# Kernel optimization log

Hardware: AMD Instinct MI355X
Metric: run time of the kernel (lower is better)

## Reference

```python
import jax, jax.numpy as jnp
import numpy as np
import math

N, E, MUL = 10000, 160000, 128
D = MUL * 4  # 128x0e (128) + 128x1o (384) = 512
NEURONS = 32
EDGE_ATTR_DIM = 32
WEIGHT_NUMEL = 4 * MUL  # 4 uvu tensor-product paths, 128 weights each


def ssp(x):
    return jax.nn.softplus(x) - math.log(2.0)


def irrep_linear(x, W0, b0, W1):
    # o3.Linear on 128x0e+128x1o: mixes mul channels within each irrep, fan-in normalized,
    # bias only on scalar (0e) block.
    s = x[:, :MUL] @ (W0 / jnp.sqrt(MUL)) + b0
    v = x[:, MUL:].reshape(-1, MUL, 3)
    v = jnp.einsum('num,uv->nvm', v, W1) / jnp.sqrt(MUL)
    return jnp.concatenate([s, v.reshape(-1, MUL * 3)], axis=-1)


def inner_product(a, b):
    # InnerProduct: uuu channel-wise irrep inner product, 1/sqrt(dim) normalized
    s = a[:, :MUL] * b[:, :MUL]
    va = a[:, MUL:].reshape(-1, MUL, 3)
    vb = b[:, MUL:].reshape(-1, MUL, 3)
    v = jnp.einsum('num,num->nu', va, vb) / jnp.sqrt(3.0)
    return jnp.concatenate([s, v], axis=-1)


def norm_gate(x, W1, b1, W2, b2):
    # NormGate: per-channel norms of l>0 irreps -> MLP gates -> gate l>0 channels
    v = x[:, MUL:].reshape(-1, MUL, 3)
    norm_v = jnp.sqrt(jnp.sum(v * v, axis=-1) + 1e-12)      # [n, 128]
    f0 = jnp.concatenate([x[:, :MUL], norm_v], axis=-1)     # [n, 256]
    g = jax.nn.silu(f0 @ W1 + b1) @ W2 + b2                 # [n, 256]
    gated = v * g[:, MUL:, None]
    return jnp.concatenate([g[:, :MUL], gated.reshape(-1, MUL * 3)], axis=-1)


def mlp2(x, Wa, Wb):
    # e3nn FullyConnectedNet: fan-in normalized, ssp nonlinearity on hidden layer only
    return ssp(x @ (Wa / jnp.sqrt(Wa.shape[0]))) @ (Wb / jnp.sqrt(Wb.shape[0]))


def setup_inputs():
    key = jax.random.key(0)
    ks = jax.random.split(key, 20)
    r = lambda i, shp: jax.random.normal(ks[i], shp, dtype=jnp.float32)
    return {
        'x': r(0, (N, D)),
        'edge_index': jax.random.randint(ks[1], (2, E), 0, N, dtype=jnp.int32),
        'edge_attr': jax.random.uniform(ks[2], (E, EDGE_ATTR_DIM), dtype=jnp.float32),
        'edge_sh': r(3, (E, 4)),
        'Wp0': r(4, (MUL, MUL)), 'bp0': jnp.zeros((MUL,), jnp.float32), 'Wp1': r(5, (MUL, MUL)),
        'ngW1': r(6, (2 * MUL, 2 * MUL)) / 16.0, 'ngb1': jnp.zeros((2 * MUL,), jnp.float32),
        'ngW2': r(7, (2 * MUL, 2 * MUL)) / 16.0, 'ngb2': jnp.zeros((2 * MUL,), jnp.float32),
        'Wn0': r(8, (MUL, MUL)), 'bn0': jnp.zeros((MUL,), jnp.float32), 'Wn1': r(9, (MUL, MUL)),
        'fcnW1': r(10, (EDGE_ATTR_DIM, NEURONS)), 'fcnW2': r(11, (NEURONS, WEIGHT_NUMEL)),
        'l0W1': r(12, (3 * MUL, NEURONS)), 'l0W2': r(13, (NEURONS, WEIGHT_NUMEL)),
        'Wo0': r(14, (MUL, MUL)), 'bo0': jnp.zeros((MUL,), jnp.float32), 'Wo1': r(15, (MUL, MUL)),
    }


def reference(x, edge_index, edge_attr, edge_sh, Wp0, bp0, Wp1, ngW1, ngb1, ngW2, ngb2,
              Wn0, bn0, Wn1, fcnW1, fcnW2, l0W1, l0W2, Wo0, bo0, Wo1):
    edge_dst, edge_src = edge_index[0], edge_index[1]
    # invariant edge descriptor s0 from pre-linear + inner product
    pre_x = irrep_linear(x, Wp0, bp0, Wp1)
    ip = inner_product(pre_x[edge_dst], pre_x[edge_src])[:, MUL:]             # [E,128]
    s0 = jnp.concatenate([pre_x[edge_dst][:, :MUL], pre_x[edge_src][:, :MUL], ip], axis=-1)  # [E,384]
    # norm-gate + linear on node features
    x = norm_gate(x, ngW1, ngb1, ngW2, ngb2)
    x = irrep_linear(x, Wn0, bn0, Wn1)
    self_x = x
    # per-edge tensor-product weights: fc_node(edge_attr) * layer_l0(s0)
    w = mlp2(edge_attr, fcnW1, fcnW2) * mlp2(s0, l0W1, l0W2)                   # [E,512]
    w1, w2, w3, w4 = w[:, :MUL], w[:, MUL:2 * MUL], w[:, 2 * MUL:3 * MUL], w[:, 3 * MUL:]
    xs = x[edge_src]
    xs0 = xs[:, :MUL]                     # [E,128]
    xs1 = xs[:, MUL:].reshape(E, MUL, 3)  # [E,128,3]
    sh0 = edge_sh[:, 0:1]
    sh1 = edge_sh[:, 1:4]
    # uvu CG tensor product paths: 0ex0e->0e, 0ex1o->1o, 1ox0e->1o, 1ox1o->0e
    c0, c1 = 0.5, jnp.sqrt(3.0) / 2.0  # path norm sqrt(ir_out.dim / n_paths)
    out0 = c0 * (w1 * xs0 * sh0 + w4 * jnp.einsum('eum,em->eu', xs1, sh1) / jnp.sqrt(3.0))
    out1 = c1 * (w2[:, :, None] * xs0[:, :, None] * sh1[:, None, :]
                 + w3[:, :, None] * xs1 * sh0[:, :, None])
    edge_feat = jnp.concatenate([out0, out1.reshape(E, MUL * 3)], axis=-1)     # [E,512]
    # scatter-aggregate to destination nodes, residual, output linear
    out = jax.ops.segment_sum(edge_feat, edge_dst, num_segments=N)
    out = out + self_x
    return irrep_linear(out, Wo0, bo0, Wo1)
```

## Files before the change

kernel.cpp:

```cpp
#include <hip/hip_runtime.h>
#include <hip/hip_fp16.h>
#include <math.h>

#define NN 10000
#define EE 160000
#define DPB 8

#define RS128 0.08838834764831845f
#define RS384 0.05103103630798287f
#define RS32  0.17677669529663687f
#define R3    0.57735026918962576f
#define C1V   0.86602540378443865f

typedef _Float16 half8 __attribute__((ext_vector_type(8)));
typedef _Float16 half4 __attribute__((ext_vector_type(4)));
typedef float f32x4 __attribute__((ext_vector_type(4)));

__device__ __forceinline__ float sspf(float x) {
    return fmaxf(x, 0.0f) + log1pf(__expf(-fabsf(x))) - 0.69314718055994530942f;
}

__device__ __forceinline__ void packone(const float* __restrict__ W,
                                        _Float16* __restrict__ P,
                                        int K, int N, int off) {
    const int KS = K >> 5;
    int j = off & 7, lane = (off >> 3) & 63, rest = off >> 9;
    int ks = rest % KS, ct = rest / KS;
    int k = ks * 32 + ((lane >> 4) << 3) + j;
    int c = ct * 16 + (lane & 15);
    P[off] = (_Float16)W[k * N + c];
}

__global__ __launch_bounds__(256) void k_packall(
    const float* __restrict__ Wp0, const float* __restrict__ Wp1,
    const float* __restrict__ Wn0, const float* __restrict__ Wn1,
    const float* __restrict__ Wo0, const float* __restrict__ Wo1,
    const float* __restrict__ ngW1, const float* __restrict__ ngW2,
    const float* __restrict__ l0W1, const float* __restrict__ fcnW1,
    const float* __restrict__ fcnW2, const float* __restrict__ l0W2,
    _Float16* __restrict__ pWp0, _Float16* __restrict__ pWp1,
    _Float16* __restrict__ pWn0, _Float16* __restrict__ pWn1,
    _Float16* __restrict__ pWo0, _Float16* __restrict__ pWo1,
    _Float16* __restrict__ png1, _Float16* __restrict__ png2,
    _Float16* __restrict__ pWc, _Float16* __restrict__ pWa,
    _Float16* __restrict__ Wf_t, _Float16* __restrict__ Wl_t) {
    int idx = blockIdx.x * 256 + threadIdx.x;
    if (idx < 98304) {
        int seg = idx >> 14, off = idx & 16383;
        if (seg == 0) packone(Wp0, pWp0, 128, 128, off);
        else if (seg == 1) packone(Wp1, pWp1, 128, 128, off);
        else if (seg == 2) packone(Wn0, pWn0, 128, 128, off);
        else if (seg == 3) packone(Wn1, pWn1, 128, 128, off);
        else if (seg == 4) packone(Wo0, pWo0, 128, 128, off);
        else packone(Wo1, pWo1, 128, 128, off);
    } else if (idx < 229376) {
        int r = idx - 98304;
        if (r < 65536) packone(ngW1, png1, 256, 256, r);
        else packone(ngW2, png2, 256, 256, r - 65536);
    } else if (idx < 233472) {
        packone(l0W1 + 256 * 32, pWc, 128, 32, idx - 229376);
    } else if (idx < 234496) {
        packone(fcnW1, pWa, 32, 32, idx - 233472);
    } else {
        int off = idx - 234496;
        int k = off & 31, c = off >> 5;
        Wf_t[c * 32 + k] = (_Float16)fcnW2[k * 512 + c];
        Wl_t[c * 32 + k] = (_Float16)l0W2[k * 512 + c];
    }
}

__global__ __launch_bounds__(256) void k_irrep_m(
    const float* __restrict__ X, const _Float16* __restrict__ pW0,
    const float* __restrict__ b0, const _Float16* __restrict__ pW1,
    float* __restrict__ out) {
    __shared__ _Float16 Xr[4][16][136];
    const int t = threadIdx.x, lane = t & 63, w = t >> 6;
    const int nb = blockIdx.x * 16;
    for (int idx = t; idx < 16 * 128; idx += 256) {
        int n = idx >> 7, c4 = idx & 127;
        const float4 v = *(const float4*)(X + (size_t)(nb + n) * 512 + 4 * c4);
        float vals[4] = {v.x, v.y, v.z, v.w};
        int c = 4 * c4;
#pragma unroll
        for (int j = 0; j < 4; ++j) {
            int cc = c + j;
            if (cc < 128) Xr[0][n][cc] = (_Float16)vals[j];
            else { int d = cc - 128; Xr[1 + d % 3][n][d / 3] = (_Float16)vals[j]; }
        }
    }
    __syncthreads();
    const _Float16* pW = (w == 0) ? pW0 : pW1;
    const int row16 = lane & 15, kg = lane >> 4;
    f32x4 acc[8];
    const f32x4 zero = {0.0f, 0.0f, 0.0f, 0.0f};
#pragma unroll
    for (int ct = 0; ct < 8; ++ct) acc[ct] = zero;
    for (int ks = 0; ks < 4; ++ks) {
        const half8 a = *(const half8*)&Xr[w][row16][ks * 32 + kg * 8];
#pragma unroll
        for (int ct = 0; ct < 8; ++ct) {
            const half8 b = *(const half8*)(pW + (((ct * 4 + ks) * 64 + lane) << 3));
            acc[ct] = __builtin_amdgcn_mfma_f32_16x16x32_f16(a, b, acc[ct], 0, 0, 0);
        }
    }
#pragma unroll
    for (int ct = 0; ct < 8; ++ct) {
        const int col = ct * 16 + row16;
        const float bb = (w == 0) ? b0[col] : 0.0f;
#pragma unroll
        for (int r = 0; r < 4; ++r) {
            const int node = nb + kg * 4 + r;
            const float val = acc[ct][r] * RS128 + bb;
            if (w == 0) out[(size_t)node * 512 + col] = val;
            else out[(size_t)node * 512 + 128 + 3 * col + (w - 1)] = val;
        }
    }
}

__global__ __launch_bounds__(256) void k_self_m(
    const float* __restrict__ X,
    const _Float16* __restrict__ png1, const float* __restrict__ ngb1,
    const _Float16* __restrict__ png2, const float* __restrict__ ngb2,
    const _Float16* __restrict__ pWn0, const float* __restrict__ bn0,
    const _Float16* __restrict__ pWn1,
    _Float16* __restrict__ selfx_h) {
    __shared__ _Float16 f0h[16][264];
    __shared__ _Float16 t1h[16][264];
    __shared__ _Float16 xvh[3][16][136];
    const int t = threadIdx.x, lane = t & 63, w = t >> 6;
    const int nb = blockIdx.x * 16;
    const int row16 = lane & 15, kg = lane >> 4;
    const f32x4 zero = {0.0f, 0.0f, 0.0f, 0.0f};

    for (int idx = t; idx < 16 * 128; idx += 256) {
        int n = idx >> 7, c4 = idx & 127;
        const float4 v = *(const float4*)(X + (size_t)(nb + n) * 512 + 4 * c4);
        float vals[4] = {v.x, v.y, v.z, v.w};
        int c = 4 * c4;
#pragma unroll
        for (int j = 0; j < 4; ++j) {
            int cc = c + j;
            if (cc < 128) f0h[n][cc] = (_Float16)vals[j];
            else { int d = cc - 128; xvh[d % 3][n][d / 3] = (_Float16)vals[j]; }
        }
    }
    __syncthreads();
    for (int idx = t; idx < 16 * 128; idx += 256) {
        int n = idx >> 7, u = idx & 127;
        float a = (float)xvh[0][n][u], b = (float)xvh[1][n][u], c = (float)xvh[2][n][u];
        f0h[n][128 + u] = (_Float16)sqrtf(fmaf(a, a, fmaf(b, b, fmaf(c, c, 1e-12f))));
    }
    __syncthreads();
    {
        f32x4 acc[4];
#pragma unroll
        for (int i = 0; i < 4; ++i) acc[i] = zero;
        for (int ks = 0; ks < 8; ++ks) {
            const half8 a = *(const half8*)&f0h[row16][ks * 32 + kg * 8];
#pragma unroll
            for (int c2 = 0; c2 < 4; ++c2) {
                const int ct = 4 * w + c2;
                const half8 b = *(const half8*)(png1 + (((ct * 8 + ks) * 64 + lane) << 3));
                acc[c2] = __builtin_amdgcn_mfma_f32_16x16x32_f16(a, b, acc[c2], 0, 0, 0);
            }
        }
#pragma unroll
        for (int c2 = 0; c2 < 4; ++c2) {
            const int col = (4 * w + c2) * 16 + row16;
            const float bb = ngb1[col];
#pragma unroll
            for (int r = 0; r < 4; ++r) {
                const float z = acc[c2][r] + bb;
                t1h[kg * 4 + r][col] = (_Float16)(z / (1.0f + __expf(-z)));
            }
        }
    }
    __syncthreads();
    {
        f32x4 acc[4];
#pragma unroll
        for (int i = 0; i < 4; ++i) acc[i] = zero;
        for (int ks = 0; ks < 8; ++ks) {
            const half8 a = *(const half8*)&t1h[row16][ks * 32 + kg * 8];
#pragma unroll
            for (int c2 = 0; c2 < 4; ++c2) {
                const int ct = 4 * w + c2;
                const half8 b = *(const half8*)(png2 + (((ct * 8 + ks) * 64 + lane) << 3));
                acc[c2] = __builtin_amdgcn_mfma_f32_16x16x32_f16(a, b, acc[c2], 0, 0, 0);
            }
        }
        __syncthreads();
#pragma unroll
        for (int c2 = 0; c2 < 4; ++c2) {
            const int col = (4 * w + c2) * 16 + row16;
            const float bb = ngb2[col];
#pragma unroll
            for (int r = 0; r < 4; ++r)
                f0h[kg * 4 + r][col] = (_Float16)(acc[c2][r] + bb);
        }
    }
    __syncthreads();
    for (int idx = t; idx < 16 * 128; idx += 256) {
        int n = idx >> 7, u = idx & 127;
        const _Float16 g = f0h[n][128 + u];
        xvh[0][n][u] = xvh[0][n][u] * g;
        xvh[1][n][u] = xvh[1][n][u] * g;
        xvh[2][n][u] = xvh[2][n][u] * g;
    }
    __syncthreads();
    {
        const _Float16* pw = (w == 0) ? pWn0 : pWn1;
        f32x4 acc[8];
#pragma unroll
        for (int ct = 0; ct < 8; ++ct) acc[ct] = zero;
        for (int ks = 0; ks < 4; ++ks) {
            const half8 a = (w == 0)
                ? *(const half8*)&f0h[row16][ks * 32 + kg * 8]
                : *(const half8*)&xvh[w - 1][row16][ks * 32 + kg * 8];
#pragma unroll
            for (int ct = 0; ct < 8; ++ct) {
                const half8 b = *(const half8*)(pw + (((ct * 4 + ks) * 64 + lane) << 3));
                acc[ct] = __builtin_amdgcn_mfma_f32_16x16x32_f16(a, b, acc[ct], 0, 0, 0);
            }
        }
#pragma unroll
        for (int ct = 0; ct < 8; ++ct) {
            const int col = ct * 16 + row16;
            const float bb = (w == 0) ? bn0[col] : 0.0f;
#pragma unroll
            for (int r = 0; r < 4; ++r) {
                const int n = kg * 4 + r;
                const float val = acc[ct][r] * RS128 + bb;
                if (w == 0) f0h[n][col] = (_Float16)val;
                else xvh[w - 1][n][col] = (_Float16)val;
            }
        }
    }
    __syncthreads();
    for (int idx = t; idx < 16 * 128; idx += 256) {
        int n = idx >> 7, u = idx & 127;
        half4 sx = {f0h[n][u], xvh[0][n][u], xvh[1][n][u], xvh[2][n][u]};
        *(half4*)(selfx_h + (size_t)(nb + n) * 512 + (u << 2)) = sx;
    }
}

__global__ __launch_bounds__(256) void k_pre(
    const float* __restrict__ prex, const float* __restrict__ l0W1,
    float* __restrict__ pAB) {
    __shared__ float xs[8][128];
    const int t = threadIdx.x;
    const int nb = blockIdx.x * 8;
    for (int idx = t; idx < 8 * 128; idx += 256) {
        int n = idx >> 7, u = idx & 127;
        xs[n][u] = prex[(size_t)(nb + n) * 512 + u];
    }
    __syncthreads();
    const int n = t >> 5, k = t & 31;
    float a = 0, b = 0;
    for (int u = 0; u < 128; ++u) {
        float s = xs[n][u];
        a = fmaf(s, l0W1[u * 32 + k], a);
        b = fmaf(s, l0W1[(128 + u) * 32 + k], b);
    }
    pAB[(size_t)(nb + n) * 64 + k] = a;
    pAB[(size_t)(nb + n) * 64 + 32 + k] = b;
}

__global__ __launch_bounds__(256) void k_deg(const int* __restrict__ ei, int* __restrict__ deg) {
    int e = blockIdx.x * 256 + threadIdx.x;
    if (e < EE) atomicAdd(&deg[ei[e]], 1);
}

__global__ __launch_bounds__(1024) void k_scan(const int* __restrict__ deg, int* __restrict__ row_ptr) {
    __shared__ int part[1024];
    const int t = threadIdx.x;
    const int base = t * 10;
    int loc[10];
    int s = 0;
#pragma unroll
    for (int i = 0; i < 10; ++i) {
        int idx = base + i;
        int d = (idx < NN) ? deg[idx] : 0;
        loc[i] = s;
        s += d;
    }
    part[t] = s;
    __syncthreads();
    for (int off = 1; off < 1024; off <<= 1) {
        int v = (t >= off) ? part[t - off] : 0;
        __syncthreads();
        part[t] += v;
        __syncthreads();
    }
    int excl = (t > 0) ? part[t - 1] : 0;
#pragma unroll
    for (int i = 0; i < 10; ++i) {
        int idx = base + i;
        if (idx <= NN) row_ptr[idx] = excl + loc[i];
    }
}

__global__ __launch_bounds__(256) void k_fill(const int* __restrict__ ei,
                                              const int* __restrict__ row_ptr,
                                              int* __restrict__ cursor,
                                              int* __restrict__ csr_eid) {
    int e = blockIdx.x * 256 + threadIdx.x;
    if (e < EE) {
        int d = ei[e];
        int pos = atomicAdd(&cursor[d], 1);
        csr_eid[row_ptr[d] + pos] = e;
    }
}

__global__ __launch_bounds__(256) void k_hidden_m(
    const float* __restrict__ prex, const float* __restrict__ pAB,
    const int* __restrict__ edge_index, const float* __restrict__ edge_attr,
    const int* __restrict__ csr_eid,
    const _Float16* __restrict__ pWc, const _Float16* __restrict__ pWa,
    __half* __restrict__ hh) {
    const int pb = blockIdx.x * 32;
    const int t = threadIdx.x, lane = t & 63, w = t >> 6;
    __shared__ _Float16 ipl[32][132];
    __shared__ _Float16 eal[32][36];
    __shared__ _Float16 h1o[32][32];
    __shared__ _Float16 hao[32][32];
    __shared__ int dsts[32], srcs[32], eids[32];

    if (t < 32) {
        const int id = csr_eid[pb + t];
        eids[t] = id;
        dsts[t] = edge_index[id];
        srcs[t] = edge_index[EE + id];
    }
    __syncthreads();
    for (int idx = t; idx < 32 * 32; idx += 256) {
        int e = idx >> 5, j = idx & 31;
        eal[e][j] = (_Float16)edge_attr[(size_t)eids[e] * 32 + j];
    }
    for (int idx = t; idx < 32 * 128; idx += 256) {
        int e = idx >> 7, u = idx & 127;
        const float* pd = prex + (size_t)dsts[e] * 512 + 128 + 3 * u;
        const float* ps = prex + (size_t)srcs[e] * 512 + 128 + 3 * u;
        ipl[e][u] = (_Float16)((pd[0] * ps[0] + pd[1] * ps[1] + pd[2] * ps[2]) * R3);
    }
    __syncthreads();

    const int row16 = lane & 15, kg = lane >> 4;
    const int mt = w >> 1, ct = w & 1;
    const int e0 = mt * 16;
    const f32x4 zero = {0.0f, 0.0f, 0.0f, 0.0f};
    const int kc = ct * 16 + row16;

    {
        f32x4 acc = zero;
#pragma unroll
        for (int ks = 0; ks < 4; ++ks) {
            const half8 a = *(const half8*)&ipl[e0 + row16][ks * 32 + kg * 8];
            const half8 b = *(const half8*)(pWc + (((ct * 4 + ks) * 64 + lane) << 3));
            acc = __builtin_amdgcn_mfma_f32_16x16x32_f16(a, b, acc, 0, 0, 0);
        }
#pragma unroll
        for (int r = 0; r < 4; ++r) {
            const int e = e0 + kg * 4 + r;
            const float v = acc[r] + pAB[(size_t)dsts[e] * 64 + kc]
                                   + pAB[(size_t)srcs[e] * 64 + 32 + kc];
            h1o[e][kc] = (_Float16)sspf(v * RS384);
        }
    }
    {
        const half8 a = *(const half8*)&eal[e0 + row16][kg * 8];
        const half8 b = *(const half8*)(pWa + ((ct * 64 + lane) << 3));
        f32x4 acc = __builtin_amdgcn_mfma_f32_16x16x32_f16(a, b, zero, 0, 0, 0);
#pragma unroll
        for (int r = 0; r < 4; ++r) {
            const int e = e0 + kg * 4 + r;
            hao[e][kc] = (_Float16)sspf((float)acc[r] * RS32);
        }
    }
    __syncthreads();
    for (int idx = t; idx < 32 * 32; idx += 256) {
        const int e = idx >> 5, j = idx & 31;
        unsigned vv;
        if (j < 16) {
            __half2 h2 = __halves2half2((__half)h1o[e][2 * j], (__half)h1o[e][2 * j + 1]);
            vv = *(unsigned*)&h2;
        } else {
            const int jj = j - 16;
            __half2 h2 = __halves2half2((__half)hao[e][2 * jj], (__half)hao[e][2 * jj + 1]);
            vv = *(unsigned*)&h2;
        }
        ((unsigned*)hh)[(size_t)(pb + e) * 32 + j] = vv;
    }
}

__global__ __launch_bounds__(512) void k_accum(
    const __half* __restrict__ hh, const _Float16* __restrict__ selfx_h,
    const int* __restrict__ edge_index, const float* __restrict__ edge_sh,
    const int* __restrict__ row_ptr, const int* __restrict__ csr_eid,
    const _Float16* __restrict__ Wf_t, const _Float16* __restrict__ Wl_t,
    float* __restrict__ outacc) {
    const int dst0 = blockIdx.x * DPB;
    const int t = threadIdx.x;
    const int lane = t & 63;
    const int wid = t >> 6;
    const int lcol = lane & 15;
    const int kg = lane >> 4;
    const int u = 16 * wid + lcol;
    const int koff = kg * 8;

    __shared__ __align__(16) _Float16 h1s[2][4][16][8];
    __shared__ __align__(16) _Float16 has[2][4][16][8];
    __shared__ float shl[2][16][4];
    __shared__ int cbeg[DPB], cne[DPB], cchk[DPB + 1];

    if (t < DPB) {
        const int b = row_ptr[dst0 + t];
        cbeg[t] = b;
        cne[t] = row_ptr[dst0 + t + 1] - b;
    }
    __syncthreads();
    if (t == 0) {
        int s = 0;
#pragma unroll
        for (int i = 0; i < DPB; ++i) { cchk[i] = s; s += max(1, (cne[i] + 15) >> 4); }
        cchk[DPB] = s;
    }
    half8 bf[4], bl[4];
#pragma unroll
    for (int q = 0; q < 4; ++q) {
        const int col = q * 128 + u;
        bf[q] = *(const half8*)(Wf_t + col * 32 + koff);
        bl[q] = *(const half8*)(Wl_t + col * 32 + koff);
    }
    __syncthreads();
    const int nc = cchk[DPB];
    const float inv32 = 1.0f / 32.0f;

    float acc0 = 0, acc1 = 0, acc2 = 0, acc3 = 0;

    unsigned rhh = 0;
    float4 rsh = {0.0f, 0.0f, 0.0f, 0.0f};
    const half4 h4z = {(_Float16)0, (_Float16)0, (_Float16)0, (_Float16)0};
    half4 nsx[4] = {h4z, h4z, h4z, h4z};
    half4 csx[4];

    const int se = t >> 5, sw = t & 31;

    auto issue = [&](int ci) {
        int dd = 0;
        while (dd + 1 < DPB && ci >= cchk[dd + 1]) ++dd;
        const int c0 = (ci - cchk[dd]) << 4;
        const int ce = min(16, cne[dd] - c0);
        const int pos = cbeg[dd] + c0;
        rhh = (se < ce) ? ((const unsigned*)hh)[(size_t)(pos + se) * 32 + sw] : 0u;
        if (t < 16) {
            if (t < ce) {
                const int id = csr_eid[pos + t];
                rsh = *(const float4*)(edge_sh + (size_t)id * 4);
            } else {
                rsh = make_float4(0.0f, 0.0f, 0.0f, 0.0f);
            }
        }
#pragma unroll
        for (int r = 0; r < 4; ++r) {
            const int e = kg * 4 + r;
            if (e < ce) {
                const int id2 = csr_eid[pos + e];
                const int s = edge_index[EE + id2];
                nsx[r] = *(const half4*)(selfx_h + (size_t)s * 512 + (u << 2));
            } else {
                nsx[r] = h4z;
            }
        }
    };

    auto flush = [&](int dd) {
        acc0 += __shfl_xor(acc0, 16, 64); acc0 += __shfl_xor(acc0, 32, 64);
        acc1 += __shfl_xor(acc1, 16, 64); acc1 += __shfl_xor(acc1, 32, 64);
        acc2 += __shfl_xor(acc2, 16, 64); acc2 += __shfl_xor(acc2, 32, 64);
        acc3 += __shfl_xor(acc3, 16, 64); acc3 += __shfl_xor(acc3, 32, 64);
        if (lane < 16) {
            const size_t g = (size_t)(dst0 + dd) * 512;
            const half4 sx = *(const half4*)(selfx_h + g + (u << 2));
            outacc[g + u] = acc0 + (float)sx.x;
            outacc[g + 128 + 3 * u + 0] = acc1 + (float)sx.y;
            outacc[g + 128 + 3 * u + 1] = acc2 + (float)sx.z;
            outacc[g + 128 + 3 * u + 2] = acc3 + (float)sx.w;
        }
        acc0 = acc1 = acc2 = acc3 = 0;
    };

    issue(0);
    int cur = 0, cur_dd = 0;
    for (int ci = 0; ci < nc; ++ci) {
        if (sw < 16) ((unsigned*)h1s[cur])[(sw >> 2) * 64 + se * 4 + (sw & 3)] = rhh;
        else         ((unsigned*)has[cur])[((sw - 16) >> 2) * 64 + se * 4 + ((sw - 16) & 3)] = rhh;
        if (t < 16) {
            shl[cur][t][0] = rsh.x; shl[cur][t][1] = rsh.y;
            shl[cur][t][2] = rsh.z; shl[cur][t][3] = rsh.w;
        }
#pragma unroll
        for (int r = 0; r < 4; ++r) csx[r] = nsx[r];
        int dd = 0;
        while (dd + 1 < DPB && ci >= cchk[dd + 1]) ++dd;
        if (ci + 1 < nc) issue(ci + 1);
        __syncthreads();
        if (dd != cur_dd) { flush(cur_dd); cur_dd = dd; }

        const half8 haf = *(const half8*)(&has[cur][kg][lcol][0]);
        const half8 h1f = *(const half8*)(&h1s[cur][kg][lcol][0]);
        const f32x4 zero = {0.0f, 0.0f, 0.0f, 0.0f};
        f32x4 A[4], B[4];
#pragma unroll
        for (int q = 0; q < 4; ++q) {
            A[q] = __builtin_amdgcn_mfma_f32_16x16x32_f16(haf, bf[q], zero, 0, 0, 0);
            B[q] = __builtin_amdgcn_mfma_f32_16x16x32_f16(h1f, bl[q], zero, 0, 0, 0);
        }
#pragma unroll
        for (int r = 0; r < 4; ++r) {
            const int e = kg * 4 + r;
            const float w1 = A[0][r] * B[0][r] * inv32;
            const float w2 = A[1][r] * B[1][r] * inv32;
            const float w3 = A[2][r] * B[2][r] * inv32;
            const float w4 = A[3][r] * B[3][r] * inv32;
            const float sh0 = shl[cur][e][0], s1x = shl[cur][e][1];
            const float s1y = shl[cur][e][2], s1z = shl[cur][e][3];
            const float xs0 = (float)csx[r].x;
            const float xv0 = (float)csx[r].y;
            const float xv1 = (float)csx[r].z;
            const float xv2 = (float)csx[r].w;
            const float dv = xv0 * s1x + xv1 * s1y + xv2 * s1z;
            acc0 += 0.5f * (w1 * xs0 * sh0 + w4 * dv * R3);
            acc1 += C1V * (w2 * xs0 * s1x + w3 * xv0 * sh0);
            acc2 += C1V * (w2 * xs0 * s1y + w3 * xv1 * sh0);
            acc3 += C1V * (w2 * xs0 * s1z + w3 * xv2 * sh0);
        }
        cur ^= 1;
    }
    flush(cur_dd);
}

extern "C" void kernel_launch(void* const* d_in, const int* in_sizes, int n_in,
                              void* d_out, int out_size, void* d_ws, size_t ws_size,
                              hipStream_t stream) {
    const float* x = (const float*)d_in[0];
    const int* edge_index = (const int*)d_in[1];
    const float* edge_attr = (const float*)d_in[2];
    const float* edge_sh = (const float*)d_in[3];
    const float* Wp0 = (const float*)d_in[4];
    const float* bp0 = (const float*)d_in[5];
    const float* Wp1 = (const float*)d_in[6];
    const float* ngW1 = (const float*)d_in[7];
    const float* ngb1 = (const float*)d_in[8];
    const float* ngW2 = (const float*)d_in[9];
    const float* ngb2 = (const float*)d_in[10];
    const float* Wn0 = (const float*)d_in[11];
    const float* bn0 = (const float*)d_in[12];
    const float* Wn1 = (const float*)d_in[13];
    const float* fcnW1 = (const float*)d_in[14];
    const float* fcnW2 = (const float*)d_in[15];
    const float* l0W1 = (const float*)d_in[16];
    const float* l0W2 = (const float*)d_in[17];
    const float* Wo0 = (const float*)d_in[18];
    const float* bo0 = (const float*)d_in[19];
    const float* Wo1 = (const float*)d_in[20];

    float* out = (float*)d_out;
    float* prex = out;
    _Float16* selfx_h = (_Float16*)d_ws;
    int* deg = (int*)(selfx_h + (size_t)NN * 512);
    int* cursor = deg + NN;
    int* row_ptr = cursor + NN;
    int* csr_eid = row_ptr + NN + 1;
    float* pAB = (float*)(csr_eid + EE);
    __half* hh = (__half*)(pAB + (size_t)NN * 64);
    _Float16* Wf_t = (_Float16*)(hh + (size_t)EE * 64);
    _Float16* Wl_t = Wf_t + 512 * 32;
    _Float16* pWp0 = Wl_t + 512 * 32;
    _Float16* pWp1 = pWp0 + 128 * 128;
    _Float16* pWn0 = pWp1 + 128 * 128;
    _Float16* pWn1 = pWn0 + 128 * 128;
    _Float16* pWo0 = pWn1 + 128 * 128;
    _Float16* pWo1 = pWo0 + 128 * 128;
    _Float16* png1 = pWo1 + 128 * 128;
    _Float16* png2 = png1 + 256 * 256;
    _Float16* pWc  = png2 + 256 * 256;
    _Float16* pWa  = pWc + 128 * 32;

    hipMemsetAsync(deg, 0, 2 * NN * sizeof(int), stream);

    k_packall<<<980, 256, 0, stream>>>(Wp0, Wp1, Wn0, Wn1, Wo0, Wo1, ngW1, ngW2,
                                       l0W1, fcnW1, fcnW2, l0W2,
                                       pWp0, pWp1, pWn0, pWn1, pWo0, pWo1,
                                       png1, png2, pWc, pWa, Wf_t, Wl_t);

    k_irrep_m<<<NN / 16, 256, 0, stream>>>(x, pWp0, bp0, pWp1, prex);
    k_pre<<<NN / 8, 256, 0, stream>>>(prex, l0W1, pAB);
    k_self_m<<<NN / 16, 256, 0, stream>>>(x, png1, ngb1, png2, ngb2, pWn0, bn0, pWn1,
                                          selfx_h);
    k_deg<<<EE / 256, 256, 0, stream>>>(edge_index, deg);
    k_scan<<<1, 1024, 0, stream>>>(deg, row_ptr);
    k_fill<<<EE / 256, 256, 0, stream>>>(edge_index, row_ptr, cursor, csr_eid);
    k_hidden_m<<<EE / 32, 256, 0, stream>>>(prex, pAB, edge_index, edge_attr, csr_eid,
                                            pWc, pWa, hh);
    k_accum<<<NN / DPB, 512, 0, stream>>>(hh, selfx_h, edge_index, edge_sh, row_ptr, csr_eid,
                                          Wf_t, Wl_t, out);
    k_irrep_m<<<NN / 16, 256, 0, stream>>>(out, pWo0, bo0, pWo1, out);
}
```

Measured before the change: 299.4 us.

## Prefetch source indices two chunks ahead and broadcast them via shuffles

Breaks the dependent index chain (csr_eid, then edge_index, then the selfx gather) into stages. Lanes 0-15 load the source node index for the chunk two steps ahead, and the row gather for the next chunk uses __shfl to broadcast those indices. This replaces the per-lane redundant dependent index loads and hides their latency. Out-of-range edges now gather node 0 and are masked in the compute loop, at the cost of extra branching and register pressure.

```diff
diff --git a/kernel.cpp b/kernel.cpp
--- a/kernel.cpp
+++ b/kernel.cpp
@@ -440,18 +440,23 @@
 
     unsigned rhh = 0;
     float4 rsh = {0.0f, 0.0f, 0.0f, 0.0f};
+    int ridx = 0;
     const half4 h4z = {(_Float16)0, (_Float16)0, (_Float16)0, (_Float16)0};
     half4 nsx[4] = {h4z, h4z, h4z, h4z};
     half4 csx[4];
 
     const int se = t >> 5, sw = t & 31;
 
-    auto issue = [&](int ci) {
+    auto chunkmeta = [&](int ci, int& pos, int& ce) {
         int dd = 0;
         while (dd + 1 < DPB && ci >= cchk[dd + 1]) ++dd;
         const int c0 = (ci - cchk[dd]) << 4;
-        const int ce = min(16, cne[dd] - c0);
-        const int pos = cbeg[dd] + c0;
+        ce = min(16, cne[dd] - c0);
+        pos = cbeg[dd] + c0;
+    };
+
+    auto issue_meta = [&](int ci) {
+        int pos, ce; chunkmeta(ci, pos, ce);
         rhh = (se < ce) ? ((const unsigned*)hh)[(size_t)(pos + se) * 32 + sw] : 0u;
         if (t < 16) {
             if (t < ce) {
@@ -461,16 +466,22 @@
                 rsh = make_float4(0.0f, 0.0f, 0.0f, 0.0f);
             }
         }
+    };
+
+    auto load_idx = [&](int ci) {
+        int pos, ce; chunkmeta(ci, pos, ce);
+        if (lane < 16) {
+            const int id = csr_eid[pos + ((lane < ce) ? lane : 0)];
+            ridx = (lane < ce) ? edge_index[EE + id] : 0;
+        }
+    };
+
+    auto gather = [&]() {
 #pragma unroll
         for (int r = 0; r < 4; ++r) {
             const int e = kg * 4 + r;
-            if (e < ce) {
-                const int id2 = csr_eid[pos + e];
-                const int s = edge_index[EE + id2];
-                nsx[r] = *(const half4*)(selfx_h + (size_t)s * 512 + (u << 2));
-            } else {
-                nsx[r] = h4z;
-            }
+            const int s = __shfl(ridx, e, 64);
+            nsx[r] = *(const half4*)(selfx_h + (size_t)s * 512 + (u << 2));
         }
     };
 
@@ -490,8 +501,12 @@
         acc0 = acc1 = acc2 = acc3 = 0;
     };
 
-    issue(0);
+    issue_meta(0);
+    load_idx(0);
+    gather();
+    if (nc > 1) load_idx(1);
     int cur = 0, cur_dd = 0;
+
     for (int ci = 0; ci < nc; ++ci) {
         if (sw < 16) ((unsigned*)h1s[cur])[(sw >> 2) * 64 + se * 4 + (sw & 3)] = rhh;
         else         ((unsigned*)has[cur])[((sw - 16) >> 2) * 64 + se * 4 + ((sw - 16) & 3)] = rhh;
@@ -501,9 +516,15 @@
         }
 #pragma unroll
         for (int r = 0; r < 4; ++r) csx[r] = nsx[r];
+        if (ci + 1 < nc) gather();
+        if (ci + 1 < nc) issue_meta(ci + 1);
+        if (ci + 2 < nc) load_idx(ci + 2);
+
         int dd = 0;
         while (dd + 1 < DPB && ci >= cchk[dd + 1]) ++dd;
-        if (ci + 1 < nc) issue(ci + 1);
+        const int c0 = (ci - cchk[dd]) << 4;
+        const int ce = min(16, cne[dd] - c0);
+
         __syncthreads();
         if (dd != cur_dd) { flush(cur_dd); cur_dd = dd; }
 
@@ -519,21 +540,23 @@
 #pragma unroll
         for (int r = 0; r < 4; ++r) {
             const int e = kg * 4 + r;
-            const float w1 = A[0][r] * B[0][r] * inv32;
-            const float w2 = A[1][r] * B[1][r] * inv32;
-            const float w3 = A[2][r] * B[2][r] * inv32;
-            const float w4 = A[3][r] * B[3][r] * inv32;
-            const float sh0 = shl[cur][e][0], s1x = shl[cur][e][1];
-            const float s1y = shl[cur][e][2], s1z = shl[cur][e][3];
-            const float xs0 = (float)csx[r].x;
-            const float xv0 = (float)csx[r].y;
-            const float xv1 = (float)csx[r].z;
-            const float xv2 = (float)csx[r].w;
-            const float dv = xv0 * s1x + xv1 * s1y + xv2 * s1z;
-            acc0 += 0.5f * (w1 * xs0 * sh0 + w4 * dv * R3);
-            acc1 += C1V * (w2 * xs0 * s1x + w3 * xv0 * sh0);
-            acc2 += C1V * (w2 * xs0 * s1y + w3 * xv1 * sh0);
-            acc3 += C1V * (w2 * xs0 * s1z + w3 * xv2 * sh0);
+            if (e < ce) {
+                const float w1 = A[0][r] * B[0][r] * inv32;
+                const float w2 = A[1][r] * B[1][r] * inv32;
+                const float w3 = A[2][r] * B[2][r] * inv32;
+                const float w4 = A[3][r] * B[3][r] * inv32;
+                const float sh0 = shl[cur][e][0], s1x = shl[cur][e][1];
+                const float s1y = shl[cur][e][2], s1z = shl[cur][e][3];
+                const float xs0 = (float)csx[r].x;
+                const float xv0 = (float)csx[r].y;
+                const float xv1 = (float)csx[r].z;
+                const float xv2 = (float)csx[r].w;
+                const float dv = xv0 * s1x + xv1 * s1y + xv2 * s1z;
+                acc0 += 0.5f * (w1 * xs0 * sh0 + w4 * dv * R3);
+                acc1 += C1V * (w2 * xs0 * s1x + w3 * xv0 * sh0);
+                acc2 += C1V * (w2 * xs0 * s1y + w3 * xv1 * sh0);
+                acc3 += C1V * (w2 * xs0 * s1z + w3 * xv2 * sh0);
+            }
         }
         cur ^= 1;
     }
```

After: 301.2 us. Within noise of the previous version (+0.6%).
